# Performance work log

Measured on AMD Instinct MI355X. Metric: run time of the kernel, lower is better.

The kernel has to match this reference:

```python
import jax, jax.numpy as jnp
import numpy as np
import math

B, C, F, W, NH = 2, 8, 1024, 512, 8
HD = F // NH


def conv2d(x, w, b):
    # NCHW 3x3 same-padding conv with bias
    y = jax.lax.conv_general_dilated(x, w, (1, 1), [(1, 1), (1, 1)],
                                     dimension_numbers=('NCHW', 'OIHW', 'NCHW'))
    return y + b[None, :, None, None]


def mc_linear(x, w):
    # per-channel linear over the feature (h) axis: (b,c,h,w) x (c,f,h) -> (b,c,f,w)
    return jnp.einsum('bchw,cfh->bcfw', x, w)


def split_heads(t):
    # (b,c,f,w) -> transpose(2,3) -> (b,c,w,f) -> (b,c,w,nh,hd) -> (b,c,nh,w,hd)
    b, c, f, w = t.shape
    return jnp.transpose(t.transpose(0, 1, 3, 2).reshape(b, c, w, NH, HD), (0, 1, 3, 2, 4))


def rotate_queries_or_keys(x):
    # lucidrains-style interleaved rotary over the sequence axis (dim -2)
    d, w = x.shape[-1], x.shape[-2]
    inv_freq = 1.0 / (10000.0 ** (jnp.arange(0, d, 2, dtype=jnp.float32) / d))
    freqs = jnp.arange(w, dtype=jnp.float32)[:, None] * inv_freq[None, :]  # (w, d/2)
    freqs = jnp.repeat(freqs, 2, axis=-1)  # (w, d)
    cos, sin = jnp.cos(freqs), jnp.sin(freqs)
    xp = x.reshape(*x.shape[:-1], d // 2, 2)
    x1, x2 = xp[..., 0], xp[..., 1]
    x_rot = jnp.stack((-x2, x1), axis=-1).reshape(x.shape)
    return x * cos + x_rot * sin


def _forward(x, prev_qk, wq_conv, bq_conv, wq_lin, wk_conv, bk_conv, wk_lin,
             wv_conv, bv_conv, wv_lin, wo_lin):
    b, c, h, w = x.shape
    q = rotate_queries_or_keys(split_heads(mc_linear(conv2d(x, wq_conv, bq_conv), wq_lin)))
    k = rotate_queries_or_keys(split_heads(mc_linear(conv2d(x, wk_conv, bk_conv), wk_lin)))
    v = split_heads(mc_linear(conv2d(x, wv_conv, bv_conv), wv_lin))
    # NOTE: original scales by sqrt(h) == sqrt(features), not sqrt(head_dim)
    qk = jnp.einsum('bcnqd,bcnkd->bcnqk', q, k) / math.sqrt(h) + prev_qk
    a = jnp.einsum('bcnqk,bcnkd->bcnqd', jax.nn.softmax(qk, axis=-1), v)
    a = jnp.transpose(a, (0, 1, 3, 2, 4)).reshape(b, c, w, h).transpose(0, 1, 3, 2)
    out = mc_linear(a, wo_lin)
    return out, qk


def setup_inputs() -> dict:
    key = jax.random.key(0)
    ks = jax.random.split(key, 10)
    s = 0.02
    return {
        'x': jax.random.normal(ks[0], (B, C, F, W), dtype=jnp.float32),
        'prev_qk': jax.random.normal(ks[1], (B, C, NH, W, W), dtype=jnp.float32) * 0.1,
        'wq_conv': jax.random.normal(ks[2], (C, C, 3, 3), dtype=jnp.float32) * s,
        'bq_conv': jnp.zeros((C,), dtype=jnp.float32),
        'wq_lin': jax.random.normal(ks[3], (C, F, F), dtype=jnp.float32) * s,
        'wk_conv': jax.random.normal(ks[4], (C, C, 3, 3), dtype=jnp.float32) * s,
        'bk_conv': jnp.zeros((C,), dtype=jnp.float32),
        'wk_lin': jax.random.normal(ks[5], (C, F, F), dtype=jnp.float32) * s,
        'wv_conv': jax.random.normal(ks[6], (C, C, 3, 3), dtype=jnp.float32) * s,
        'bv_conv': jnp.zeros((C,), dtype=jnp.float32),
        'wv_lin': jax.random.normal(ks[7], (C, F, F), dtype=jnp.float32) * s,
        'wo_lin': jax.random.normal(ks[8], (C, F, F), dtype=jnp.float32) * s,
    }


def reference(x, prev_qk, wq_conv, bq_conv, wq_lin, wk_conv, bk_conv, wk_lin,
              wv_conv, bv_conv, wv_lin, wo_lin):
    return _forward(x, prev_qk, wq_conv, bq_conv, wq_lin, wk_conv, bk_conv, wk_lin,
                    wv_conv, bv_conv, wv_lin, wo_lin)
```

## Files before the change

### kernel.cpp

```cpp
#include <hip/hip_runtime.h>
#include <stdint.h>


typedef float f32x4 __attribute__((ext_vector_type(4)));
typedef short s16x8 __attribute__((ext_vector_type(8)));

__device__ __forceinline__ short f2bf(float f) {
  union { float f; uint32_t u; } v; v.f = f;
  uint32_t r = v.u + 0x7FFFu + ((v.u >> 16) & 1u);
  return (short)(r >> 16);
}

__device__ __forceinline__ void g2l16(const void* g, void* l) {
  __builtin_amdgcn_global_load_lds(
      (const __attribute__((address_space(1))) void*)g,
      (__attribute__((address_space(3))) void*)l, 16, 0, 0);
}

__device__ __forceinline__ void gemm_core(const short* __restrict__ A,
                                          const short* __restrict__ B,
                                          int K, short* sA, short* sB,
                                          f32x4 (*acc)[4]) {
  const int tid = threadIdx.x;
  const int lane = tid & 63;
  const int wv = tid >> 6;
  const int wm = wv >> 1, wn = wv & 1;
  const int q = lane >> 4, cix = lane & 15;

  for (int k0 = 0; k0 < K; k0 += 32) {
    __syncthreads();
#pragma unroll
    for (int i = 0; i < 2; ++i) {
      int seg = wv + 4 * i;
      int m = seg * 16 + (lane >> 2);
      int ko = (lane & 3) * 8;
      g2l16(B + (size_t)m * K + k0 + ko, sB + seg * 512);
    }
#pragma unroll
    for (int i = 0; i < 2; ++i) {
      int seg = wv + 4 * i;
      int m = seg * 16 + (lane >> 2);
      int ko = (lane & 3) * 8;
      g2l16(A + (size_t)m * K + k0 + ko, sA + seg * 512);
    }
    __syncthreads();
    s16x8 afr[4], bfr[4];
#pragma unroll
    for (int i = 0; i < 4; ++i)
      afr[i] = *(const s16x8*)(sA + (wm * 64 + i * 16 + cix) * 32 + q * 8);
#pragma unroll
    for (int i = 0; i < 4; ++i)
      bfr[i] = *(const s16x8*)(sB + (wn * 64 + i * 16 + cix) * 32 + q * 8);
#pragma unroll
    for (int i = 0; i < 4; ++i)
#pragma unroll
      for (int j = 0; j < 4; ++j)
        acc[i][j] = __builtin_amdgcn_mfma_f32_16x16x32_bf16(afr[i], bfr[j],
                                                            acc[i][j], 0, 0, 0);
  }
}

__global__ void __launch_bounds__(256) k_cvt(
    const float* __restrict__ w0, const float* __restrict__ w1,
    const float* __restrict__ w2, const float* __restrict__ w3,
    short* __restrict__ Wb) {
  size_t i = (size_t)blockIdx.x * 256 + threadIdx.x;
#pragma unroll
  for (int r = 0; r < 4; ++r) {
    const float* s = (r == 0) ? w0 : (r == 1) ? w1 : (r == 2) ? w2 : w3;
    size_t v = i + (size_t)r * 2097152;
    float4 f = *(const float4*)(s + (i << 2));
    short4 o;
    o.x = f2bf(f.x); o.y = f2bf(f.y); o.z = f2bf(f.z); o.w = f2bf(f.w);
    *(short4*)(Wb + (v << 2)) = o;
  }
}

__global__ void __launch_bounds__(256) k_conv(
    const float* __restrict__ x,
    const float* __restrict__ wqc, const float* __restrict__ bqc,
    const float* __restrict__ wkc, const float* __restrict__ bkc,
    const float* __restrict__ wvc, const float* __restrict__ bvc,
    short* __restrict__ Yt) {
  __shared__ float xs[8][66][19];
  const int h0 = blockIdx.x * 64, w0 = blockIdx.y * 16, b = blockIdx.z;
  const int tid = threadIdx.x;
  for (int idx = tid; idx < 8 * 66 * 18; idx += 256) {
    int c = idx / (66 * 18);
    int rem = idx % (66 * 18);
    int r = rem / 18, cc = rem % 18;
    int h = h0 + r - 1, w = w0 + cc - 1;
    float v = 0.f;
    if (h >= 0 && h < 1024 && w >= 0 && w < 512)
      v = x[(((size_t)b * 8 + c) << 10 | (unsigned)h) * 512 + w];
    xs[c][r][cc] = v;
  }
  __syncthreads();
  const int hh = tid & 63;
  const int wv4 = tid >> 6;
  const size_t hgl = h0 + hh;
  for (int proj = 0; proj < 3; ++proj) {
    const float* wc = (proj == 0) ? wqc : ((proj == 1) ? wkc : wvc);
    const float* bc = (proj == 0) ? bqc : ((proj == 1) ? bkc : bvc);
    float a[4][8];
#pragma unroll
    for (int jj = 0; jj < 4; ++jj)
#pragma unroll
      for (int co = 0; co < 8; ++co) a[jj][co] = bc[co];
    for (int ci = 0; ci < 8; ++ci)
#pragma unroll
      for (int dh = 0; dh < 3; ++dh)
#pragma unroll
        for (int dw = 0; dw < 3; ++dw) {
          float xv[4];
#pragma unroll
          for (int jj = 0; jj < 4; ++jj)
            xv[jj] = xs[ci][hh + dh][wv4 * 4 + jj + dw];
          const int wi = ci * 9 + dh * 3 + dw;
#pragma unroll
          for (int co = 0; co < 8; ++co) {
            float wgt = wc[co * 72 + wi];
#pragma unroll
            for (int jj = 0; jj < 4; ++jj) a[jj][co] = fmaf(xv[jj], wgt, a[jj][co]);
          }
        }
#pragma unroll
    for (int jj = 0; jj < 4; ++jj) {
      size_t col = (size_t)b * 512 + w0 + wv4 * 4 + jj;
#pragma unroll
      for (int co = 0; co < 8; ++co)
        Yt[((size_t)(proj * 8 + co) << 20) + (col << 10) + hgl] = f2bf(a[jj][co]);
    }
  }
}

__global__ void __launch_bounds__(256) k_qkv(
    const short* __restrict__ Wb, const short* __restrict__ Yt,
    short* __restrict__ Qr, short* __restrict__ Kr, short* __restrict__ Vt) {
  __shared__ short sA[128 * 32], sB[128 * 32];
  const int L = blockIdx.x;
  const int lin = (L & 7) * 192 + (L >> 3);
  const int g = lin >> 6;
  const int t = lin & 63;
  const int proj = g >> 3, cq = g & 7;
  const int mt = t >> 3, nt = t & 7;
  const short* A = Wb + ((size_t)g << 20) + ((size_t)mt << 17);
  const short* B = Yt + ((size_t)g << 20) + ((size_t)nt << 17);
  const f32x4 fzero = {0.f, 0.f, 0.f, 0.f};
  f32x4 acc[4][4];
#pragma unroll
  for (int i = 0; i < 4; ++i)
#pragma unroll
    for (int j = 0; j < 4; ++j) acc[i][j] = fzero;
  gemm_core(A, B, 1024, sA, sB, acc);

  const int lane = threadIdx.x & 63, wv = threadIdx.x >> 6;
  const int wm = wv >> 1, wn = wv & 1, q = lane >> 4, cix = lane & 15;
  const int head = mt;
  if (proj == 2) {
#pragma unroll
    for (int mi = 0; mi < 4; ++mi) {
      int rbase = wm * 64 + mi * 16 + q * 4;
#pragma unroll
      for (int ni = 0; ni < 4; ++ni) {
        int col = nt * 128 + wn * 64 + ni * 16 + cix;
        int b = col >> 9, wpos = col & 511;
        size_t base = ((size_t)((cq * 8 + head) * 2 + b) << 16) +
                      ((size_t)rbase << 9) + wpos;
        f32x4 v = acc[mi][ni];
        Vt[base] = f2bf(v[0]);
        Vt[base + 512] = f2bf(v[1]);
        Vt[base + 1024] = f2bf(v[2]);
        Vt[base + 1536] = f2bf(v[3]);
      }
    }
  } else {
    short* QKp = proj ? Kr : Qr;
#pragma unroll
    for (int mi = 0; mi < 4; ++mi) {
      int rbase = wm * 64 + mi * 16 + q * 4;
      int j0 = rbase >> 1;
      float if0 = exp2f(-0.20762050593046f * (float)j0);
      float if1 = exp2f(-0.20762050593046f * (float)(j0 + 1));
#pragma unroll
      for (int ni = 0; ni < 4; ++ni) {
        int col = nt * 128 + wn * 64 + ni * 16 + cix;
        int b = col >> 9, wpos = col & 511;
        float fw = (float)wpos;
        float s0, c0, s1, c1;
        __sincosf(fw * if0, &s0, &c0);
        __sincosf(fw * if1, &s1, &c1);
        f32x4 v = acc[mi][ni];
        short4 pk;
        pk.x = f2bf(v[0] * c0 - v[1] * s0);
        pk.y = f2bf(v[1] * c0 + v[0] * s0);
        pk.z = f2bf(v[2] * c1 - v[3] * s1);
        pk.w = f2bf(v[3] * c1 + v[2] * s1);
        *(short4*)&QKp[((size_t)(((cq * 8 + head) * 2 + b) * 512 + wpos) << 7) +
                       rbase] = pk;
      }
    }
  }
}

__global__ void __launch_bounds__(256, 3) k_attn(
    const short* __restrict__ Qr, const short* __restrict__ Kr,
    const short* __restrict__ Vt, const float* __restrict__ prevqk,
    float* __restrict__ qk, short* __restrict__ At) {
  __shared__ short Pt[128 * 136];
  __shared__ float psum[128][2];
  const int tid = threadIdx.x, lane = tid & 63, wv = tid >> 6;
  const int wm = wv >> 1, wn = wv & 1, q = lane >> 4, cix = lane & 15;
  const int bid = blockIdx.x;
  const int lin = (bid & 7) * 64 + (bid >> 3);
  const int bcn = lin >> 2, qt = lin & 3;
  const int b = bcn >> 6, cch = (bcn >> 3) & 7, nh = bcn & 7;
  const size_t qrb = ((size_t)((cch * 8 + nh) * 2 + b)) << 16;
  const size_t rowg0 = (size_t)bcn * 512 + qt * 128;
  const int arow = wm * 64;
  const short* Qbase = Qr + qrb + ((size_t)qt << 14);

  const f32x4 fzero = {0.f, 0.f, 0.f, 0.f};
  f32x4 accO[4][4];
  float lsum[4][4];
#pragma unroll
  for (int i = 0; i < 4; ++i)
#pragma unroll
    for (int j = 0; j < 4; ++j) { accO[i][j] = fzero; lsum[i][j] = 0.f; }

  float pvA[8], pvB[8];

#pragma unroll 1
  for (int kt = 0; kt < 4; ++kt) {
    const int colb = kt * 128 + wn * 64 + cix;
    f32x4 accS[4][4];
#pragma unroll
    for (int i = 0; i < 4; ++i)
#pragma unroll
      for (int j = 0; j < 4; ++j) accS[i][j] = fzero;

    auto ld8 = [&](int mi, int h, float* dst) {
#pragma unroll
      for (int u = 0; u < 2; ++u)
#pragma unroll
        for (int r = 0; r < 4; ++r)
          dst[u * 4 + r] =
              prevqk[((rowg0 + arow + mi * 16 + q * 4 + r) << 9) +
                     colb + (2 * h + u) * 16];
    };
    auto pr8 = [&](int mi, int h, const float* pv) {
#pragma unroll
      for (int u = 0; u < 2; ++u) {
        int ni = 2 * h + u;
#pragma unroll
        for (int r = 0; r < 4; ++r) {
          float s = accS[mi][ni][r] * 0.03125f + pv[u * 4 + r];
          qk[((rowg0 + arow + mi * 16 + q * 4 + r) << 9) + colb + ni * 16] = s;
          float p = __expf(s);
          lsum[mi][r] += p;
          Pt[(arow + mi * 16 + q * 4 + r) * 136 + wn * 64 + ni * 16 + cix] =
              f2bf(p);
        }
      }
    };

    ld8(0, 0, pvA);

    const short* Kbase = Kr + qrb + ((size_t)kt << 14);
#pragma unroll
    for (int kk = 0; kk < 4; ++kk) {
      s16x8 afr[4];
#pragma unroll
      for (int mi = 0; mi < 4; ++mi)
        afr[mi] = *(const s16x8*)(Qbase +
            ((size_t)(arow + mi * 16 + cix) << 7) + kk * 32 + q * 8);
      __builtin_amdgcn_s_setprio(1);
#pragma unroll
      for (int ni = 0; ni < 4; ++ni) {
        s16x8 bfr = *(const s16x8*)(Kbase +
            ((size_t)(wn * 64 + ni * 16 + cix) << 7) + kk * 32 + q * 8);
#pragma unroll
        for (int mi = 0; mi < 4; ++mi)
          accS[mi][ni] = __builtin_amdgcn_mfma_f32_16x16x32_bf16(
              afr[mi], bfr, accS[mi][ni], 0, 0, 0);
      }
      __builtin_amdgcn_s_setprio(0);
    }

    ld8(0, 1, pvB); pr8(0, 0, pvA);
    ld8(1, 0, pvA); pr8(0, 1, pvB);
    ld8(1, 1, pvB); pr8(1, 0, pvA);
    ld8(2, 0, pvA); pr8(1, 1, pvB);
    ld8(2, 1, pvB); pr8(2, 0, pvA);
    ld8(3, 0, pvA); pr8(2, 1, pvB);
    ld8(3, 1, pvB); pr8(3, 0, pvA);
    pr8(3, 1, pvB);

    __syncthreads();

#pragma unroll
    for (int s4 = 0; s4 < 4; ++s4) {
      s16x8 afr[4];
#pragma unroll
      for (int i = 0; i < 4; ++i)
        afr[i] =
            *(const s16x8*)&Pt[(arow + i * 16 + cix) * 136 + s4 * 32 + q * 8];
      __builtin_amdgcn_s_setprio(1);
#pragma unroll
      for (int j = 0; j < 4; ++j) {
        s16x8 bfr = *(const s16x8*)&Vt[qrb +
                                       ((size_t)(wn * 64 + j * 16 + cix) << 9) +
                                       kt * 128 + s4 * 32 + q * 8];
#pragma unroll
        for (int i = 0; i < 4; ++i)
          accO[i][j] = __builtin_amdgcn_mfma_f32_16x16x32_bf16(
              afr[i], bfr, accO[i][j], 0, 0, 0);
      }
      __builtin_amdgcn_s_setprio(0);
    }
    __syncthreads();
  }

#pragma unroll
  for (int mi = 0; mi < 4; ++mi)
#pragma unroll
    for (int r = 0; r < 4; ++r) {
      float se = lsum[mi][r];
      se += __shfl_xor(se, 1);
      se += __shfl_xor(se, 2);
      se += __shfl_xor(se, 4);
      se += __shfl_xor(se, 8);
      if (cix == 0) psum[arow + mi * 16 + q * 4 + r][wn] = se;
    }
  __syncthreads();
#pragma unroll
  for (int mi = 0; mi < 4; ++mi) {
    int rl = arow + mi * 16 + q * 4;
    float iL[4];
#pragma unroll
    for (int r = 0; r < 4; ++r)
      iL[r] = 1.0f / (psum[rl + r][0] + psum[rl + r][1]);
    int wq = qt * 128 + rl;
#pragma unroll
    for (int ni = 0; ni < 4; ++ni) {
      int dl = wn * 64 + ni * 16 + cix;
      size_t ob = (((size_t)cch << 10) + b * 512 + wq) * 1024 + nh * 128 + dl;
      f32x4 v = accO[mi][ni];
      At[ob] = f2bf(v[0] * iL[0]);
      At[ob + 1024] = f2bf(v[1] * iL[1]);
      At[ob + 2048] = f2bf(v[2] * iL[2]);
      At[ob + 3072] = f2bf(v[3] * iL[3]);
    }
  }
}

__global__ void __launch_bounds__(256) k_out(
    const short* __restrict__ At, const short* __restrict__ Wob,
    float* __restrict__ outp) {
  __shared__ short sA[128 * 32], sB[128 * 32];
  const int L = blockIdx.x;
  const int lin = (L & 7) * 64 + (L >> 3);
  const int c = lin >> 6;
  const int t = lin & 63;
  const int mt = t >> 3, nt = t & 7;
  const short* A = At + ((size_t)c << 20) + ((size_t)mt << 17);
  const short* B = Wob + ((size_t)c << 20) + ((size_t)nt << 17);
  const f32x4 fzero = {0.f, 0.f, 0.f, 0.f};
  f32x4 acc[4][4];
#pragma unroll
  for (int i = 0; i < 4; ++i)
#pragma unroll
    for (int j = 0; j < 4; ++j) acc[i][j] = fzero;
  gemm_core(A, B, 1024, sA, sB, acc);

  const int lane = threadIdx.x & 63, wv = threadIdx.x >> 6;
  const int wm = wv >> 1, wn = wv & 1, q = lane >> 4, cix = lane & 15;
#pragma unroll
  for (int mi = 0; mi < 4; ++mi) {
    int colm = mt * 128 + wm * 64 + mi * 16 + q * 4;
    int b = colm >> 9, w = colm & 511;
#pragma unroll
    for (int ni = 0; ni < 4; ++ni) {
      int f = nt * 128 + wn * 64 + ni * 16 + cix;
      f32x4 v = acc[mi][ni];
      float4 st; st.x = v[0]; st.y = v[1]; st.z = v[2]; st.w = v[3];
      *(float4*)&outp[((((size_t)b * 8 + c) << 10) + f) * 512 + w] = st;
    }
  }
}

extern "C" void kernel_launch(void* const* d_in, const int* in_sizes, int n_in,
                              void* d_out, int out_size, void* d_ws,
                              size_t ws_size, hipStream_t stream) {
  const float* x = (const float*)d_in[0];
  const float* prevqk = (const float*)d_in[1];
  const float* wqc = (const float*)d_in[2];
  const float* bqc = (const float*)d_in[3];
  const float* wql = (const float*)d_in[4];
  const float* wkc = (const float*)d_in[5];
  const float* bkc = (const float*)d_in[6];
  const float* wkl = (const float*)d_in[7];
  const float* wvc = (const float*)d_in[8];
  const float* bvc = (const float*)d_in[9];
  const float* wvl = (const float*)d_in[10];
  const float* wol = (const float*)d_in[11];
  float* outp = (float*)d_out;
  float* qk = outp + 8388608;

  char* ws = (char*)d_ws;
  short* Wb = (short*)ws;
  short* Yt = (short*)(ws + 67108864);
  short* Qr = (short*)(ws + 117440512);
  short* Kr = (short*)(ws + 134217728);
  short* Vt = (short*)(ws + 150994944);
  short* At = (short*)(ws + 67108864);
  short* Wob = Wb + ((size_t)24 << 20);

  k_cvt<<<dim3(8192), 256, 0, stream>>>(wql, wkl, wvl, wol, Wb);
  k_conv<<<dim3(16, 32, 2), 256, 0, stream>>>(x, wqc, bqc, wkc, bkc, wvc, bvc, Yt);
  k_qkv<<<dim3(1536), 256, 0, stream>>>(Wb, Yt, Qr, Kr, Vt);
  k_attn<<<dim3(512), 256, 0, stream>>>(Qr, Kr, Vt, prevqk, qk, At);
  k_out<<<dim3(512), 256, 0, stream>>>(At, Wob, outp);
}
```

Measured before the change: 670.6 us.

## Double-buffer GEMM LDS staging and split attention score tile into halves

The shared GEMM core now ping-pongs between two LDS buffers, issuing the global-to-LDS loads for the next K slice before computing the current one and keeping one barrier per iteration instead of two. The QKV and output kernels double their shared arrays to hold both buffers. Separately, the attention kernel computes the QK^T score tile in two halves of 32 columns, so only 8 score accumulators are live at a time instead of 16, which lowers register pressure. This costs more LDS per block, which can reduce occupancy, and the attention kernel reloads Q fragments for each half.

```diff
diff --git a/kernel.cpp b/kernel.cpp
--- a/kernel.cpp
+++ b/kernel.cpp
@@ -26,37 +26,48 @@
   const int wv = tid >> 6;
   const int wm = wv >> 1, wn = wv & 1;
   const int q = lane >> 4, cix = lane & 15;
-
-  for (int k0 = 0; k0 < K; k0 += 32) {
-    __syncthreads();
+  const int mrow = lane >> 2;
+  const int ko8 = (lane & 3) * 8;
+
+  auto stage = [&](int k0, int buf) {
+    short* dA = sA + buf * 4096;
+    short* dB = sB + buf * 4096;
 #pragma unroll
     for (int i = 0; i < 2; ++i) {
       int seg = wv + 4 * i;
-      int m = seg * 16 + (lane >> 2);
-      int ko = (lane & 3) * 8;
-      g2l16(B + (size_t)m * K + k0 + ko, sB + seg * 512);
+      int m = seg * 16 + mrow;
+      g2l16(B + (size_t)m * K + k0 + ko8, dB + seg * 512);
     }
 #pragma unroll
     for (int i = 0; i < 2; ++i) {
       int seg = wv + 4 * i;
-      int m = seg * 16 + (lane >> 2);
-      int ko = (lane & 3) * 8;
-      g2l16(A + (size_t)m * K + k0 + ko, sA + seg * 512);
-    }
-    __syncthreads();
+      int m = seg * 16 + mrow;
+      g2l16(A + (size_t)m * K + k0 + ko8, dA + seg * 512);
+    }
+  };
+
+  stage(0, 0);
+  __syncthreads();
+  int buf = 0;
+  for (int k0 = 0; k0 < K; k0 += 32) {
+    if (k0 + 32 < K) stage(k0 + 32, buf ^ 1);
+    const short* cA = sA + buf * 4096;
+    const short* cB = sB + buf * 4096;
     s16x8 afr[4], bfr[4];
 #pragma unroll
     for (int i = 0; i < 4; ++i)
-      afr[i] = *(const s16x8*)(sA + (wm * 64 + i * 16 + cix) * 32 + q * 8);
+      afr[i] = *(const s16x8*)(cA + (wm * 64 + i * 16 + cix) * 32 + q * 8);
 #pragma unroll
     for (int i = 0; i < 4; ++i)
-      bfr[i] = *(const s16x8*)(sB + (wn * 64 + i * 16 + cix) * 32 + q * 8);
+      bfr[i] = *(const s16x8*)(cB + (wn * 64 + i * 16 + cix) * 32 + q * 8);
 #pragma unroll
     for (int i = 0; i < 4; ++i)
 #pragma unroll
       for (int j = 0; j < 4; ++j)
         acc[i][j] = __builtin_amdgcn_mfma_f32_16x16x32_bf16(afr[i], bfr[j],
                                                             acc[i][j], 0, 0, 0);
+    __syncthreads();
+    buf ^= 1;
   }
 }
 
@@ -137,7 +148,7 @@
 __global__ void __launch_bounds__(256) k_qkv(
     const short* __restrict__ Wb, const short* __restrict__ Yt,
     short* __restrict__ Qr, short* __restrict__ Kr, short* __restrict__ Vt) {
-  __shared__ short sA[128 * 32], sB[128 * 32];
+  __shared__ short sA[2 * 128 * 32], sB[2 * 128 * 32];
   const int L = blockIdx.x;
   const int lin = (L & 7) * 192 + (L >> 3);
   const int g = lin >> 6;
@@ -233,68 +244,68 @@
 #pragma unroll 1
   for (int kt = 0; kt < 4; ++kt) {
     const int colb = kt * 128 + wn * 64 + cix;
-    f32x4 accS[4][4];
-#pragma unroll
-    for (int i = 0; i < 4; ++i)
-#pragma unroll
-      for (int j = 0; j < 4; ++j) accS[i][j] = fzero;
-
-    auto ld8 = [&](int mi, int h, float* dst) {
-#pragma unroll
-      for (int u = 0; u < 2; ++u)
-#pragma unroll
-        for (int r = 0; r < 4; ++r)
-          dst[u * 4 + r] =
-              prevqk[((rowg0 + arow + mi * 16 + q * 4 + r) << 9) +
-                     colb + (2 * h + u) * 16];
-    };
-    auto pr8 = [&](int mi, int h, const float* pv) {
-#pragma unroll
-      for (int u = 0; u < 2; ++u) {
-        int ni = 2 * h + u;
-#pragma unroll
-        for (int r = 0; r < 4; ++r) {
-          float s = accS[mi][ni][r] * 0.03125f + pv[u * 4 + r];
-          qk[((rowg0 + arow + mi * 16 + q * 4 + r) << 9) + colb + ni * 16] = s;
-          float p = __expf(s);
-          lsum[mi][r] += p;
-          Pt[(arow + mi * 16 + q * 4 + r) * 136 + wn * 64 + ni * 16 + cix] =
-              f2bf(p);
+    const short* Kbase = Kr + qrb + ((size_t)kt << 14);
+
+#pragma unroll 1
+    for (int h2 = 0; h2 < 2; ++h2) {
+      f32x4 accS[4][2];
+#pragma unroll
+      for (int i = 0; i < 4; ++i) { accS[i][0] = fzero; accS[i][1] = fzero; }
+
+      auto ld8 = [&](int mi, float* dst) {
+#pragma unroll
+        for (int u = 0; u < 2; ++u)
+#pragma unroll
+          for (int r = 0; r < 4; ++r)
+            dst[u * 4 + r] =
+                prevqk[((rowg0 + arow + mi * 16 + q * 4 + r) << 9) +
+                       colb + (2 * h2 + u) * 16];
+      };
+      auto pr8 = [&](int mi, const float* pv) {
+#pragma unroll
+        for (int u = 0; u < 2; ++u) {
+          int ni = 2 * h2 + u;
+#pragma unroll
+          for (int r = 0; r < 4; ++r) {
+            float s = accS[mi][u][r] * 0.03125f + pv[u * 4 + r];
+            qk[((rowg0 + arow + mi * 16 + q * 4 + r) << 9) + colb + ni * 16] =
+                s;
+            float p = __expf(s);
+            lsum[mi][r] += p;
+            Pt[(arow + mi * 16 + q * 4 + r) * 136 + wn * 64 + ni * 16 + cix] =
+                f2bf(p);
+          }
         }
+      };
+
+      ld8(0, pvA);
+
+#pragma unroll
+      for (int kk = 0; kk < 4; ++kk) {
+        s16x8 bfr[2];
+#pragma unroll
+        for (int u = 0; u < 2; ++u)
+          bfr[u] = *(const s16x8*)(Kbase +
+              ((size_t)(wn * 64 + (2 * h2 + u) * 16 + cix) << 7) +
+              kk * 32 + q * 8);
+        __builtin_amdgcn_s_setprio(1);
+#pragma unroll
+        for (int mi = 0; mi < 4; ++mi) {
+          s16x8 afr = *(const s16x8*)(Qbase +
+              ((size_t)(arow + mi * 16 + cix) << 7) + kk * 32 + q * 8);
+          accS[mi][0] = __builtin_amdgcn_mfma_f32_16x16x32_bf16(
+              afr, bfr[0], accS[mi][0], 0, 0, 0);
+          accS[mi][1] = __builtin_amdgcn_mfma_f32_16x16x32_bf16(
+              afr, bfr[1], accS[mi][1], 0, 0, 0);
+        }
+        __builtin_amdgcn_s_setprio(0);
       }
-    };
-
-    ld8(0, 0, pvA);
-
-    const short* Kbase = Kr + qrb + ((size_t)kt << 14);
-#pragma unroll
-    for (int kk = 0; kk < 4; ++kk) {
-      s16x8 afr[4];
-#pragma unroll
-      for (int mi = 0; mi < 4; ++mi)
-        afr[mi] = *(const s16x8*)(Qbase +
-            ((size_t)(arow + mi * 16 + cix) << 7) + kk * 32 + q * 8);
-      __builtin_amdgcn_s_setprio(1);
-#pragma unroll
-      for (int ni = 0; ni < 4; ++ni) {
-        s16x8 bfr = *(const s16x8*)(Kbase +
-            ((size_t)(wn * 64 + ni * 16 + cix) << 7) + kk * 32 + q * 8);
-#pragma unroll
-        for (int mi = 0; mi < 4; ++mi)
-          accS[mi][ni] = __builtin_amdgcn_mfma_f32_16x16x32_bf16(
-              afr[mi], bfr, accS[mi][ni], 0, 0, 0);
-      }
-      __builtin_amdgcn_s_setprio(0);
-    }
-
-    ld8(0, 1, pvB); pr8(0, 0, pvA);
-    ld8(1, 0, pvA); pr8(0, 1, pvB);
-    ld8(1, 1, pvB); pr8(1, 0, pvA);
-    ld8(2, 0, pvA); pr8(1, 1, pvB);
-    ld8(2, 1, pvB); pr8(2, 0, pvA);
-    ld8(3, 0, pvA); pr8(2, 1, pvB);
-    ld8(3, 1, pvB); pr8(3, 0, pvA);
-    pr8(3, 1, pvB);
+
+      ld8(1, pvB); pr8(0, pvA);
+      ld8(2, pvA); pr8(1, pvB);
+      ld8(3, pvB); pr8(2, pvA);
+      pr8(3, pvB);
+    }
 
     __syncthreads();
 
@@ -357,7 +368,7 @@
 __global__ void __launch_bounds__(256) k_out(
     const short* __restrict__ At, const short* __restrict__ Wob,
     float* __restrict__ outp) {
-  __shared__ short sA[128 * 32], sB[128 * 32];
+  __shared__ short sA[2 * 128 * 32], sB[2 * 128 * 32];
   const int L = blockIdx.x;
   const int lin = (L & 7) * 64 + (L >> 3);
   const int c = lin >> 6;
```

After: 695.9 us. 3.8% more time.
